# Optimization experiments

Hardware: AMD Instinct MI355X
Metric: run time of the kernel (lower is better)

## Reference

```python
import jax, jax.numpy as jnp
import numpy as np


def setup_inputs() -> dict:
    key = jax.random.key(0)
    k1, k2, k3 = jax.random.split(key, 3)
    B, Lc, Lq, D = 32, 1024, 128, 1024
    context_features = jax.random.normal(k1, (B, Lc, D), dtype=jnp.float32)
    question_features = jax.random.normal(k2, (B, Lq, D), dtype=jnp.float32)
    # weight of nn.Linear(3*D, 1, bias=False): shape (3*D,), split into w1,w2,w3
    w = jax.random.normal(k3, (3 * D,), dtype=jnp.float32) * (1.0 / np.sqrt(3 * D))
    return {"context_features": context_features, "question_features": question_features, "w": w}


def reference(context_features, question_features, w):
    B, Lc, D = context_features.shape
    Lq = question_features.shape[1]
    w1, w2, w3 = w[:D], w[D:2 * D], w[2 * D:]
    # Trilinear similarity: sim[b,i,j] = w1.c_i + w2.q_j + w3.(c_i*q_j)
    # Decomposed so the (B,Lc,Lq,3D) concat tensor is never materialized.
    sim = (
        jnp.einsum("bcd,d->bc", context_features, w1)[:, :, None]      # [B,Lc,1]
        + jnp.einsum("bqd,d->bq", question_features, w2)[:, None, :]    # [B,1,Lq]
        + jnp.einsum("bcd,bqd->bcq", context_features * w3, question_features)
    )  # [B,Lc,Lq]
    # context-to-question attention
    c2q = jnp.einsum("bcq,bqd->bcd", jax.nn.softmax(sim, axis=2), question_features)
    # question-to-context attention
    b = jax.nn.softmax(jnp.max(sim, axis=2), axis=-1)                   # [B,Lc]
    q2c = jnp.einsum("bc,bcd->bd", b, context_features)                 # [B,D]
    q2c = jnp.broadcast_to(q2c[:, None, :], (B, Lc, D))                 # repeat over Lc
    return (c2q, q2c)
```

## Files before the change

kernel.cpp:

```cpp
#include <hip/hip_runtime.h>
#include <hip/hip_bf16.h>
#include <stdint.h>

#define B_  32
#define LC  1024
#define LQ  128
#define DD  1024
#define CT  64
#define BK  64

typedef __attribute__((ext_vector_type(8))) short short8;
typedef __attribute__((ext_vector_type(4))) float f4;
typedef unsigned short u16;

__device__ __forceinline__ u16 f2bf(float f) {
  __hip_bfloat16 h = __float2bfloat16(f);
  return *reinterpret_cast<u16*>(&h);
}

__device__ __forceinline__ void gld16(const u16* g, void* l) {
  __builtin_amdgcn_global_load_lds(
      (const __attribute__((address_space(1))) unsigned int*)g,
      (__attribute__((address_space(3))) unsigned int*)l,
      16, 0, 0);
}

__device__ __forceinline__ void barrier_vm4() {
  __builtin_amdgcn_sched_barrier(0);
  asm volatile("s_waitcnt vmcnt(4) lgkmcnt(0)" ::: "memory");
  __builtin_amdgcn_s_barrier();
  __builtin_amdgcn_sched_barrier(0);
}

__global__ __launch_bounds__(256) void k1m(const float* __restrict__ qf,
                                           const float* __restrict__ w,
                                           u16* __restrict__ qw3_bf,
                                           u16* __restrict__ qT_bf,
                                           float* __restrict__ qwpart) {
  __shared__ float w3s[128];
  __shared__ float w2s[128];
  __shared__ __align__(16) u16 ldsq[128][136];
  int blk = blockIdx.x;
  int b = blk >> 3, dt = blk & 7;
  int t = threadIdx.x;
  if (t < 128) { w3s[t] = w[2 * DD + dt * 128 + t]; w2s[t] = w[DD + dt * 128 + t]; }
  __syncthreads();
  {
    int q = t >> 1, half = t & 1;
    const float* src = qf + (size_t)(b * LQ + q) * DD + dt * 128 + half * 64;
    u16* dst = qw3_bf + (size_t)(b * LQ + q) * DD + dt * 128 + half * 64;
    float s2 = 0.f;
    #pragma unroll
    for (int j = 0; j < 8; ++j) {
      float4 a = *(const float4*)(src + j * 8);
      float4 c = *(const float4*)(src + j * 8 + 4);
      float vals[8] = {a.x, a.y, a.z, a.w, c.x, c.y, c.z, c.w};
      u16 u3[8] __attribute__((aligned(16)));
      #pragma unroll
      for (int jj = 0; jj < 8; ++jj) {
        int dl = half * 64 + j * 8 + jj;
        s2 += vals[jj] * w2s[dl];
        u3[jj] = f2bf(vals[jj] * w3s[dl]);
        ldsq[dl][q] = f2bf(vals[jj]);
      }
      *(short8*)(dst + j * 8) = *(short8*)u3;
    }
    s2 += __shfl_xor(s2, 1);
    if (half == 0) qwpart[(size_t)(b * 8 + dt) * LQ + q] = s2;
  }
  __syncthreads();
  {
    int d = t >> 1, qh = (t & 1) * 64;
    u16* gdst = qT_bf + (size_t)b * DD * LQ + (size_t)(dt * 128 + d) * LQ + qh;
    #pragma unroll
    for (int i = 0; i < 8; ++i) {
      short8 v = *(const short8*)(&ldsq[d][qh + i * 8]);
      *(short8*)(gdst + i * 8) = v;
    }
  }
}

__device__ __forceinline__ void stage3(const u16* aqT, int dt,
                                       unsigned char* qbase, int wv, int lane) {
  #pragma unroll
  for (int i = 0; i < 4; ++i) {
    unsigned rel = wv * 4096 + i * 1024 + lane * 16;
    int r = rel >> 8, c = (rel >> 4) & 15, cs = c ^ (r & 7);
    gld16(aqT + (size_t)(dt * 64 + r) * LQ + cs * 8, qbase + wv * 4096 + i * 1024);
  }
}

#define STAGEB_PH1(K0, BUF)                                                    \
  do {                                                                         \
    _Pragma("unroll")                                                          \
    for (int i_ = 0; i_ < 4; ++i_) {                                           \
      unsigned rel_ = wv * 4096 + i_ * 1024 + lane * 16;                       \
      int r_ = rel_ >> 7, c_ = (rel_ >> 4) & 7, cs_ = c_ ^ (r_ & 7);           \
      gld16(aq3 + (size_t)r_ * DD + (K0) + cs_ * 8,                            \
            (BUF) + 8192 + wv * 4096 + i_ * 1024);                             \
    }                                                                          \
  } while (0)

#define LOADCTX_PH1(VA, K0)                                                    \
  do {                                                                         \
    const float* s_ = actx + (size_t)ar * DD + (K0) + akc;                     \
    *(float4*)(VA)      = *(const float4*)(s_);                                \
    *(float4*)(VA + 4)  = *(const float4*)(s_ + 4);                            \
    *(float4*)(VA + 8)  = *(const float4*)(s_ + 8);                            \
    *(float4*)(VA + 12) = *(const float4*)(s_ + 12);                           \
  } while (0)

#define CWWRITE_PH1(VA, K0, BUF)                                               \
  do {                                                                         \
    _Pragma("unroll")                                                          \
    for (int j_ = 0; j_ < 4; ++j_) {                                           \
      float4 w4_ = *(const float4*)(&w1s[(K0) + akc + j_ * 4]);                \
      cwp += (VA)[j_ * 4 + 0] * w4_.x + (VA)[j_ * 4 + 1] * w4_.y +             \
             (VA)[j_ * 4 + 2] * w4_.z + (VA)[j_ * 4 + 3] * w4_.w;              \
    }                                                                          \
    {                                                                          \
      u16 u_[16] __attribute__((aligned(16)));                                 \
      _Pragma("unroll")                                                        \
      for (int j_ = 0; j_ < 16; ++j_) u_[j_] = f2bf((VA)[j_]);                 \
      int cu_ = akc >> 3;                                                      \
      *(short8*)((BUF) + ar * 128 + ((cu_ ^ (ar & 7)) << 4)) = *(short8*)u_;   \
      *(short8*)((BUF) + ar * 128 + (((cu_ + 1) ^ (ar & 7)) << 4)) =           \
          *(short8*)(u_ + 8);                                                  \
    }                                                                          \
  } while (0)

#define MFMA_PH1(BUFC)                                                         \
  do {                                                                         \
    _Pragma("unroll")                                                          \
    for (int kk = 0; kk < 2; ++kk) {                                           \
      short8 afr[2], bfr[4];                                                   \
      _Pragma("unroll")                                                        \
      for (int m_ = 0; m_ < 2; ++m_) {                                         \
        int r_ = wr * 32 + m_ * 16 + l15;                                      \
        int byte_ = r_ * 128 + kk * 64 + l4 * 16;                              \
        byte_ ^= (r_ & 7) << 4;                                                \
        afr[m_] = *(const short8*)((BUFC) + byte_);                            \
      }                                                                        \
      _Pragma("unroll")                                                        \
      for (int n_ = 0; n_ < 4; ++n_) {                                         \
        int r_ = wc * 64 + n_ * 16 + l15;                                      \
        int byte_ = r_ * 128 + kk * 64 + l4 * 16;                              \
        byte_ ^= (r_ & 7) << 4;                                                \
        bfr[n_] = *(const short8*)((BUFC) + 8192 + byte_);                     \
      }                                                                        \
      _Pragma("unroll")                                                        \
      for (int m_ = 0; m_ < 2; ++m_)                                           \
        _Pragma("unroll")                                                      \
        for (int n_ = 0; n_ < 4; ++n_)                                         \
          acc[m_][n_] = __builtin_amdgcn_mfma_f32_16x16x32_bf16(               \
              afr[m_], bfr[n_], acc[m_][n_], 0, 0, 0);                         \
    }                                                                          \
  } while (0)

#define PH1_ITER(T, VA_WR, VA_LD, BUFC, BUFN)                                  \
  do {                                                                         \
    STAGEB_PH1(((T) + 1) * BK, BUFN);                                          \
    __builtin_amdgcn_sched_barrier(0);                                         \
    LOADCTX_PH1(VA_LD, ((T) + 2) * BK);                                        \
    MFMA_PH1(BUFC);                                                            \
    CWWRITE_PH1(VA_WR, ((T) + 1) * BK, BUFN);                                  \
    barrier_vm4();                                                             \
  } while (0)

__global__ __launch_bounds__(256, 2) void kA(const float* __restrict__ ctx,
                                          const u16* __restrict__ qw3_bf,
                                          const u16* __restrict__ qT_bf,
                                          const float* __restrict__ w,
                                          const float* __restrict__ qwpart,
                                          float* __restrict__ c2q,
                                          float* __restrict__ partial,
                                          float* __restrict__ tileM,
                                          float* __restrict__ tileS) {
  __shared__ __align__(16) unsigned char tile[49152];
  __shared__ __align__(16) float w1s[DD];
  __shared__ float cws[CT];
  __shared__ float qws[LQ];
  __shared__ float rm2[2][CT];
  __shared__ float rs2[2][CT];
  __shared__ float rmax[CT];
  __shared__ float rinv[CT];
  __shared__ float wgtl[CT];

  unsigned char* psm = tile + 32768;

  const int tid = threadIdx.x;
  const int bid = blockIdx.x;
  const int blk = (bid & 7) * 64 + (bid >> 3);
  const int b   = blk >> 4;
  const int c0  = (blk & 15) * CT;
  const int lane = tid & 63;
  const int wv   = tid >> 6;
  const int wr   = wv >> 1;
  const int wc   = wv & 1;
  const int l15  = lane & 15;
  const int l4   = lane >> 4;

  *(f4*)(&w1s[tid * 4]) = *(const f4*)(w + tid * 4);
  if (tid < LQ) {
    float s = 0.f;
    #pragma unroll
    for (int dt = 0; dt < 8; ++dt) s += qwpart[(size_t)(b * 8 + dt) * LQ + tid];
    qws[tid] = s;
  }

  f4 acc[2][4];
  #pragma unroll
  for (int m = 0; m < 2; ++m)
    #pragma unroll
    for (int n = 0; n < 4; ++n) { f4 z = {0.f, 0.f, 0.f, 0.f}; acc[m][n] = z; }

  const float* actx = ctx + (size_t)(b * LC + c0) * DD;
  const u16* aq3  = qw3_bf + (size_t)b * LQ * DD;
  const u16* aqT  = qT_bf + (size_t)b * DD * LQ;

  const int ar  = tid >> 2;
  const int akc = (tid & 3) * 16;

  float vaA[16], vaB[16];
  float cwp = 0.f;

  __syncthreads();

  {
    LOADCTX_PH1(vaA, 0);
    __builtin_amdgcn_sched_barrier(0);
    STAGEB_PH1(0, tile);
    __builtin_amdgcn_sched_barrier(0);
    CWWRITE_PH1(vaA, 0, tile);
    LOADCTX_PH1(vaB, BK);
    barrier_vm4();
  }

  for (int t2 = 0; t2 < 7; ++t2) {
    PH1_ITER(2 * t2,     vaB, vaA, tile,         tile + 24576);
    PH1_ITER(2 * t2 + 1, vaA, vaB, tile + 24576, tile);
  }
  {
    STAGEB_PH1(15 * BK, tile + 24576);
    MFMA_PH1(tile);
    CWWRITE_PH1(vaB, 15 * BK, tile + 24576);
    __syncthreads();
  }
  MFMA_PH1(tile + 24576);
  __syncthreads();

  cwp += __shfl_xor(cwp, 1);
  cwp += __shfl_xor(cwp, 2);
  if ((lane & 3) == 0) cws[ar] = cwp;
  __syncthreads();

  #pragma unroll
  for (int m = 0; m < 2; ++m) {
    #pragma unroll
    for (int j = 0; j < 4; ++j) {
      int cl = wr * 32 + m * 16 + l4 * 4 + j;
      float mx = -1e30f;
      #pragma unroll
      for (int n = 0; n < 4; ++n) {
        float v = acc[m][n][j] + cws[cl] + qws[wc * 64 + n * 16 + l15];
        acc[m][n][j] = v;
        mx = fmaxf(mx, v);
      }
      #pragma unroll
      for (int off = 1; off < 16; off <<= 1) mx = fmaxf(mx, __shfl_xor(mx, off));
      if (l15 == 0) rm2[wc][cl] = mx;
    }
  }
  __syncthreads();
  if (tid < CT) rmax[tid] = fmaxf(rm2[0][tid], rm2[1][tid]);
  __syncthreads();
  #pragma unroll
  for (int m = 0; m < 2; ++m) {
    #pragma unroll
    for (int j = 0; j < 4; ++j) {
      int cl = wr * 32 + m * 16 + l4 * 4 + j;
      float mx = rmax[cl];
      float s = 0.f;
      #pragma unroll
      for (int n = 0; n < 4; ++n) {
        float p = __expf(acc[m][n][j] - mx);
        s += p;
        int q = wc * 64 + n * 16 + l15;
        int byte = cl * (LQ * 2) + q * 2;
        byte ^= (cl & 7) << 4;
        *(u16*)(psm + byte) = f2bf(p);
      }
      #pragma unroll
      for (int off = 1; off < 16; off <<= 1) s += __shfl_xor(s, off);
      if (l15 == 0) rs2[wc][cl] = s;
    }
  }
  __syncthreads();
  if (tid < CT) {
    rinv[tid] = 1.f / (rs2[0][tid] + rs2[1][tid]);
    float m = rmax[tid];
    float M = m;
    #pragma unroll
    for (int off = 32; off; off >>= 1) M = fmaxf(M, __shfl_xor(M, off));
    float wq = __expf(m - M);
    wgtl[tid] = wq;
    float S = wq;
    #pragma unroll
    for (int off = 32; off; off >>= 1) S += __shfl_xor(S, off);
    if (tid == 0) { tileM[blk] = M; tileS[blk] = S; }
  }
  __syncthreads();

  stage3(aqT, 0, tile, wv, lane);
  __syncthreads();

  float ri[2];
  ri[0] = rinv[wr * 32 + l15];
  ri[1] = rinv[wr * 32 + 16 + l15];

  f4 pacc25 = {0.f, 0.f, 0.f, 0.f};
  const float* pbase = actx + tid * 4;

  for (int dt = 0; dt < 16; ++dt) {
    int cur = dt & 1;
    if (dt < 15) stage3(aqT, dt + 1, tile + (cur ^ 1) * 16384, wv, lane);
    #pragma unroll
    for (int cc = 0; cc < 4; ++cc) {
      int c = dt * 4 + cc;
      pacc25 += wgtl[c] * *(const f4*)(pbase + (size_t)c * DD);
    }
    unsigned char* qbase = tile + cur * 16384;
    f4 pacc[2][2];
    #pragma unroll
    for (int n = 0; n < 2; ++n)
      #pragma unroll
      for (int m = 0; m < 2; ++m) { f4 z = {0.f, 0.f, 0.f, 0.f}; pacc[n][m] = z; }
    #pragma unroll
    for (int kk = 0; kk < 4; ++kk) {
      short8 pa[2], qb[2];
      #pragma unroll
      for (int m = 0; m < 2; ++m) {
        int r = wr * 32 + m * 16 + l15;
        int byte = r * 256 + kk * 64 + l4 * 16;
        byte ^= (r & 7) << 4;
        pa[m] = *(const short8*)(psm + byte);
      }
      #pragma unroll
      for (int n = 0; n < 2; ++n) {
        int dl = wc * 32 + n * 16 + l15;
        int byte = dl * 256 + kk * 64 + l4 * 16;
        byte ^= (dl & 7) << 4;
        qb[n] = *(const short8*)(qbase + byte);
      }
      #pragma unroll
      for (int n = 0; n < 2; ++n)
        #pragma unroll
        for (int m = 0; m < 2; ++m)
          pacc[n][m] = __builtin_amdgcn_mfma_f32_16x16x32_bf16(qb[n], pa[m], pacc[n][m], 0, 0, 0);
    }
    #pragma unroll
    for (int n = 0; n < 2; ++n)
      #pragma unroll
      for (int m = 0; m < 2; ++m) {
        f4 v = pacc[n][m] * ri[m];
        int cl = wr * 32 + m * 16 + l15;
        int dc = wc * 32 + n * 16 + l4 * 4;
        *(f4*)(c2q + (size_t)(b * LC + c0 + cl) * DD + dt * 64 + dc) = v;
      }
    __syncthreads();
  }

  *(f4*)(partial + (size_t)blk * DD + tid * 4) = pacc25;
}

__global__ __launch_bounds__(256) void kQC2(const float* __restrict__ partial,
                                            const float* __restrict__ tileM,
                                            const float* __restrict__ tileS,
                                            float* __restrict__ out2) {
  int blk = blockIdx.x;
  int b = blk >> 5, cb = blk & 31;
  int t = threadIdx.x;
  __shared__ float sc[16];
  __shared__ float dninv;
  if (t < 16) {
    float m = tileM[b * 16 + t];
    float M = m;
    #pragma unroll
    for (int off = 8; off; off >>= 1) M = fmaxf(M, __shfl_xor(M, off));
    float e = __expf(m - M);
    sc[t] = e;
    float d = e * tileS[b * 16 + t];
    #pragma unroll
    for (int off = 8; off; off >>= 1) d += __shfl_xor(d, off);
    if (t == 0) dninv = 1.f / d;
  }
  __syncthreads();
  f4 a = {0.f, 0.f, 0.f, 0.f};
  #pragma unroll
  for (int i = 0; i < 16; ++i) {
    float s = sc[i];
    f4 v = *(const f4*)(partial + (size_t)(b * 16 + i) * DD + t * 4);
    a += s * v;
  }
  a *= dninv;
  float* dst = out2 + ((size_t)b * LC + cb * 32) * DD + t * 4;
  #pragma unroll
  for (int r = 0; r < 32; ++r) *(f4*)(dst + (size_t)r * DD) = a;
}

extern "C" void kernel_launch(void* const* d_in, const int* in_sizes, int n_in,
                              void* d_out, int out_size, void* d_ws, size_t ws_size,
                              hipStream_t stream) {
  (void)in_sizes; (void)n_in; (void)out_size; (void)ws_size;
  const float* ctx = (const float*)d_in[0];
  const float* qf  = (const float*)d_in[1];
  const float* w   = (const float*)d_in[2];
  float* out      = (float*)d_out;
  float* c2q      = out;
  float* q2c_out  = out + (size_t)B_ * LC * DD;

  float* ws     = (float*)d_ws;
  float* qwpart = ws;
  float* tileM  = qwpart + B_ * 8 * LQ;
  float* tileS  = tileM + 512;
  float* part   = tileS + 512;
  u16*   qw3_bf = (u16*)(part + 512 * DD);
  u16*   qT_bf  = qw3_bf + (size_t)B_ * LQ * DD;

  hipLaunchKernelGGL(k1m,  dim3(256),  dim3(256), 0, stream, qf, w, qw3_bf, qT_bf, qwpart);
  hipLaunchKernelGGL(kA,   dim3(512),  dim3(256), 0, stream, ctx, qw3_bf, qT_bf, w, qwpart, c2q, part, tileM, tileS);
  hipLaunchKernelGGL(kQC2, dim3(1024), dim3(256), 0, stream, part, tileM, tileS, q2c_out);
}
```

Baseline: 136.4 us.

## Split fused attention kernel into similarity kernel and separate PV matmul kernel

```diff
diff --git a/kernel.cpp b/kernel.cpp
--- a/kernel.cpp
+++ b/kernel.cpp
@@ -23,13 +23,6 @@
       (const __attribute__((address_space(1))) unsigned int*)g,
       (__attribute__((address_space(3))) unsigned int*)l,
       16, 0, 0);
-}
-
-__device__ __forceinline__ void barrier_vm4() {
-  __builtin_amdgcn_sched_barrier(0);
-  asm volatile("s_waitcnt vmcnt(4) lgkmcnt(0)" ::: "memory");
-  __builtin_amdgcn_s_barrier();
-  __builtin_amdgcn_sched_barrier(0);
 }
 
 __global__ __launch_bounds__(256) void k1m(const float* __restrict__ qf,
@@ -77,16 +70,6 @@
       short8 v = *(const short8*)(&ldsq[d][qh + i * 8]);
       *(short8*)(gdst + i * 8) = v;
     }
-  }
-}
-
-__device__ __forceinline__ void stage3(const u16* aqT, int dt,
-                                       unsigned char* qbase, int wv, int lane) {
-  #pragma unroll
-  for (int i = 0; i < 4; ++i) {
-    unsigned rel = wv * 4096 + i * 1024 + lane * 16;
-    int r = rel >> 8, c = (rel >> 4) & 15, cs = c ^ (r & 7);
-    gld16(aqT + (size_t)(dt * 64 + r) * LQ + cs * 8, qbase + wv * 4096 + i * 1024);
   }
 }
 
@@ -157,22 +140,12 @@
     }                                                                          \
   } while (0)
 
-#define PH1_ITER(T, VA_WR, VA_LD, BUFC, BUFN)                                  \
-  do {                                                                         \
-    STAGEB_PH1(((T) + 1) * BK, BUFN);                                          \
-    __builtin_amdgcn_sched_barrier(0);                                         \
-    LOADCTX_PH1(VA_LD, ((T) + 2) * BK);                                        \
-    MFMA_PH1(BUFC);                                                            \
-    CWWRITE_PH1(VA_WR, ((T) + 1) * BK, BUFN);                                  \
-    barrier_vm4();                                                             \
-  } while (0)
-
-__global__ __launch_bounds__(256, 2) void kA(const float* __restrict__ ctx,
+__global__ __launch_bounds__(256, 2) void kSim(const float* __restrict__ ctx,
                                           const u16* __restrict__ qw3_bf,
-                                          const u16* __restrict__ qT_bf,
                                           const float* __restrict__ w,
                                           const float* __restrict__ qwpart,
-                                          float* __restrict__ c2q,
+                                          u16* __restrict__ Pg,
+                                          float* __restrict__ rinvg,
                                           float* __restrict__ partial,
                                           float* __restrict__ tileM,
                                           float* __restrict__ tileS) {
@@ -216,38 +189,36 @@
 
   const float* actx = ctx + (size_t)(b * LC + c0) * DD;
   const u16* aq3  = qw3_bf + (size_t)b * LQ * DD;
-  const u16* aqT  = qT_bf + (size_t)b * DD * LQ;
 
   const int ar  = tid >> 2;
   const int akc = (tid & 3) * 16;
 
-  float vaA[16], vaB[16];
+  float va[16];
   float cwp = 0.f;
 
   __syncthreads();
 
   {
-    LOADCTX_PH1(vaA, 0);
+    LOADCTX_PH1(va, 0);
     __builtin_amdgcn_sched_barrier(0);
     STAGEB_PH1(0, tile);
     __builtin_amdgcn_sched_barrier(0);
-    CWWRITE_PH1(vaA, 0, tile);
-    LOADCTX_PH1(vaB, BK);
-    barrier_vm4();
-  }
-
-  for (int t2 = 0; t2 < 7; ++t2) {
-    PH1_ITER(2 * t2,     vaB, vaA, tile,         tile + 24576);
-    PH1_ITER(2 * t2 + 1, vaA, vaB, tile + 24576, tile);
-  }
-  {
-    STAGEB_PH1(15 * BK, tile + 24576);
-    MFMA_PH1(tile);
-    CWWRITE_PH1(vaB, 15 * BK, tile + 24576);
+    CWWRITE_PH1(va, 0, tile);
+  }
+  __syncthreads();
+
+  for (int t = 0; t < 16; ++t) {
+    int cur = t & 1;
+    unsigned char* bufc = tile + cur * 24576;
+    unsigned char* bufn = tile + (cur ^ 1) * 24576;
+    if (t < 15) {
+      LOADCTX_PH1(va, (t + 1) * BK);
+      STAGEB_PH1((t + 1) * BK, bufn);
+    }
+    MFMA_PH1(bufc);
+    if (t < 15) CWWRITE_PH1(va, (t + 1) * BK, bufn);
     __syncthreads();
   }
-  MFMA_PH1(tile + 24576);
-  __syncthreads();
 
   cwp += __shfl_xor(cwp, 1);
   cwp += __shfl_xor(cwp, 2);
@@ -311,66 +282,90 @@
   }
   __syncthreads();
 
-  stage3(aqT, 0, tile, wv, lane);
-  __syncthreads();
+  if (tid < CT) rinvg[blk * CT + tid] = rinv[tid];
+
+  {
+    int row = tid >> 2, chunk = tid & 3;
+    u16* pg = Pg + (size_t)blk * (CT * LQ) + row * LQ + chunk * 32;
+    #pragma unroll
+    for (int j = 0; j < 4; ++j) {
+      int col16 = chunk * 4 + j;
+      int sb = row * 256 + ((col16 ^ (row & 7)) << 4);
+      short8 v = *(const short8*)(psm + sb);
+      *(short8*)(pg + j * 8) = v;
+    }
+  }
+
+  {
+    f4 pacc25 = {0.f, 0.f, 0.f, 0.f};
+    const float* pbase = actx + tid * 4;
+    #pragma unroll 8
+    for (int c = 0; c < CT; ++c)
+      pacc25 += wgtl[c] * *(const f4*)(pbase + (size_t)c * DD);
+    *(f4*)(partial + (size_t)blk * DD + tid * 4) = pacc25;
+  }
+}
+
+__global__ __launch_bounds__(256, 3) void kPV(const u16* __restrict__ Pg,
+                                              const u16* __restrict__ qT_bf,
+                                              const float* __restrict__ rinvg,
+                                              float* __restrict__ c2q) {
+  const int tid = threadIdx.x;
+  const int bid = blockIdx.x;
+  const int lb  = (bid & 7) * 512 + (bid >> 3);
+  const int blk = lb >> 3;
+  const int dch = lb & 7;
+  const int b   = blk >> 4;
+  const int c0  = (blk & 15) * CT;
+  const int lane = tid & 63;
+  const int wv   = tid >> 6;
+  const int wr   = wv >> 1;
+  const int wd   = wv & 1;
+  const int l15  = lane & 15;
+  const int l4   = lane >> 4;
+
+  const u16* pt  = Pg + (size_t)blk * (CT * LQ);
+  const u16* qb0 = qT_bf + (size_t)b * DD * LQ;
 
   float ri[2];
-  ri[0] = rinv[wr * 32 + l15];
-  ri[1] = rinv[wr * 32 + 16 + l15];
-
-  f4 pacc25 = {0.f, 0.f, 0.f, 0.f};
-  const float* pbase = actx + tid * 4;
-
-  for (int dt = 0; dt < 16; ++dt) {
-    int cur = dt & 1;
-    if (dt < 15) stage3(aqT, dt + 1, tile + (cur ^ 1) * 16384, wv, lane);
-    #pragma unroll
-    for (int cc = 0; cc < 4; ++cc) {
-      int c = dt * 4 + cc;
-      pacc25 += wgtl[c] * *(const f4*)(pbase + (size_t)c * DD);
-    }
-    unsigned char* qbase = tile + cur * 16384;
-    f4 pacc[2][2];
-    #pragma unroll
-    for (int n = 0; n < 2; ++n)
-      #pragma unroll
-      for (int m = 0; m < 2; ++m) { f4 z = {0.f, 0.f, 0.f, 0.f}; pacc[n][m] = z; }
-    #pragma unroll
-    for (int kk = 0; kk < 4; ++kk) {
-      short8 pa[2], qb[2];
-      #pragma unroll
-      for (int m = 0; m < 2; ++m) {
-        int r = wr * 32 + m * 16 + l15;
-        int byte = r * 256 + kk * 64 + l4 * 16;
-        byte ^= (r & 7) << 4;
-        pa[m] = *(const short8*)(psm + byte);
-      }
-      #pragma unroll
-      for (int n = 0; n < 2; ++n) {
-        int dl = wc * 32 + n * 16 + l15;
-        int byte = dl * 256 + kk * 64 + l4 * 16;
-        byte ^= (dl & 7) << 4;
-        qb[n] = *(const short8*)(qbase + byte);
-      }
-      #pragma unroll
-      for (int n = 0; n < 2; ++n)
-        #pragma unroll
-        for (int m = 0; m < 2; ++m)
-          pacc[n][m] = __builtin_amdgcn_mfma_f32_16x16x32_bf16(qb[n], pa[m], pacc[n][m], 0, 0, 0);
-    }
-    #pragma unroll
-    for (int n = 0; n < 2; ++n)
-      #pragma unroll
-      for (int m = 0; m < 2; ++m) {
-        f4 v = pacc[n][m] * ri[m];
-        int cl = wr * 32 + m * 16 + l15;
-        int dc = wc * 32 + n * 16 + l4 * 4;
-        *(f4*)(c2q + (size_t)(b * LC + c0 + cl) * DD + dt * 64 + dc) = v;
-      }
-    __syncthreads();
-  }
-
-  *(f4*)(partial + (size_t)blk * DD + tid * 4) = pacc25;
+  ri[0] = rinvg[blk * CT + wr * 32 + l15];
+  ri[1] = rinvg[blk * CT + wr * 32 + 16 + l15];
+
+  f4 pacc[4][2];
+  #pragma unroll
+  for (int n = 0; n < 4; ++n)
+    #pragma unroll
+    for (int m = 0; m < 2; ++m) { f4 z = {0.f, 0.f, 0.f, 0.f}; pacc[n][m] = z; }
+
+  #pragma unroll
+  for (int kk = 0; kk < 4; ++kk) {
+    short8 pa[2], qb[4];
+    #pragma unroll
+    for (int m = 0; m < 2; ++m) {
+      int r = wr * 32 + m * 16 + l15;
+      pa[m] = *(const short8*)(pt + (size_t)r * LQ + kk * 32 + l4 * 8);
+    }
+    #pragma unroll
+    for (int n = 0; n < 4; ++n) {
+      int dl = dch * 128 + wd * 64 + n * 16 + l15;
+      qb[n] = *(const short8*)(qb0 + (size_t)dl * LQ + kk * 32 + l4 * 8);
+    }
+    #pragma unroll
+    for (int n = 0; n < 4; ++n)
+      #pragma unroll
+      for (int m = 0; m < 2; ++m)
+        pacc[n][m] = __builtin_amdgcn_mfma_f32_16x16x32_bf16(qb[n], pa[m], pacc[n][m], 0, 0, 0);
+  }
+
+  #pragma unroll
+  for (int n = 0; n < 4; ++n)
+    #pragma unroll
+    for (int m = 0; m < 2; ++m) {
+      f4 v = pacc[n][m] * ri[m];
+      int cl = wr * 32 + m * 16 + l15;
+      int dc = dch * 128 + wd * 64 + n * 16 + l4 * 4;
+      *(f4*)(c2q + (size_t)(b * LC + c0 + cl) * DD + dc) = v;
+    }
 }
 
 __global__ __launch_bounds__(256) void kQC2(const float* __restrict__ partial,
@@ -423,11 +418,14 @@
   float* qwpart = ws;
   float* tileM  = qwpart + B_ * 8 * LQ;
   float* tileS  = tileM + 512;
-  float* part   = tileS + 512;
+  float* rinvg  = tileS + 512;
+  float* part   = rinvg + 512 * CT;
   u16*   qw3_bf = (u16*)(part + 512 * DD);
   u16*   qT_bf  = qw3_bf + (size_t)B_ * LQ * DD;
+  u16*   Pg     = qT_bf + (size_t)B_ * DD * LQ;
 
   hipLaunchKernelGGL(k1m,  dim3(256),  dim3(256), 0, stream, qf, w, qw3_bf, qT_bf, qwpart);
-  hipLaunchKernelGGL(kA,   dim3(512),  dim3(256), 0, stream, ctx, qw3_bf, qT_bf, w, qwpart, c2q, part, tileM, tileS);
+  hipLaunchKernelGGL(kSim, dim3(512),  dim3(256), 0, stream, ctx, qw3_bf, w, qwpart, Pg, rinvg, part, tileM, tileS);
+  hipLaunchKernelGGL(kPV,  dim3(4096), dim3(256), 0, stream, Pg, qT_bf, rinvg, c2q);
   hipLaunchKernelGGL(kQC2, dim3(1024), dim3(256), 0, stream, part, tileM, tileS, q2c_out);
 }
```

Result: slower. 160.1 us (+17.4%).

## Load context A fragments directly into MFMA registers, skipping LDS staging

Applied to the files above, without the earlier changes.

```diff
diff --git a/kernel.cpp b/kernel.cpp
--- a/kernel.cpp
+++ b/kernel.cpp
@@ -23,13 +23,6 @@
       (const __attribute__((address_space(1))) unsigned int*)g,
       (__attribute__((address_space(3))) unsigned int*)l,
       16, 0, 0);
-}
-
-__device__ __forceinline__ void barrier_vm4() {
-  __builtin_amdgcn_sched_barrier(0);
-  asm volatile("s_waitcnt vmcnt(4) lgkmcnt(0)" ::: "memory");
-  __builtin_amdgcn_s_barrier();
-  __builtin_amdgcn_sched_barrier(0);
 }
 
 __global__ __launch_bounds__(256) void k1m(const float* __restrict__ qf,
@@ -90,84 +83,73 @@
   }
 }
 
-#define STAGEB_PH1(K0, BUF)                                                    \
+#define STAGEB(K0, BUF)                                                        \
   do {                                                                         \
     _Pragma("unroll")                                                          \
     for (int i_ = 0; i_ < 4; ++i_) {                                           \
       unsigned rel_ = wv * 4096 + i_ * 1024 + lane * 16;                       \
       int r_ = rel_ >> 7, c_ = (rel_ >> 4) & 7, cs_ = c_ ^ (r_ & 7);           \
       gld16(aq3 + (size_t)r_ * DD + (K0) + cs_ * 8,                            \
-            (BUF) + 8192 + wv * 4096 + i_ * 1024);                             \
+            (BUF) + wv * 4096 + i_ * 1024);                                    \
     }                                                                          \
   } while (0)
 
-#define LOADCTX_PH1(VA, K0)                                                    \
-  do {                                                                         \
-    const float* s_ = actx + (size_t)ar * DD + (K0) + akc;                     \
-    *(float4*)(VA)      = *(const float4*)(s_);                                \
-    *(float4*)(VA + 4)  = *(const float4*)(s_ + 4);                            \
-    *(float4*)(VA + 8)  = *(const float4*)(s_ + 8);                            \
-    *(float4*)(VA + 12) = *(const float4*)(s_ + 12);                           \
-  } while (0)
-
-#define CWWRITE_PH1(VA, K0, BUF)                                               \
+#define ALOAD(K0)                                                              \
   do {                                                                         \
     _Pragma("unroll")                                                          \
-    for (int j_ = 0; j_ < 4; ++j_) {                                           \
-      float4 w4_ = *(const float4*)(&w1s[(K0) + akc + j_ * 4]);                \
-      cwp += (VA)[j_ * 4 + 0] * w4_.x + (VA)[j_ * 4 + 1] * w4_.y +             \
-             (VA)[j_ * 4 + 2] * w4_.z + (VA)[j_ * 4 + 3] * w4_.w;              \
-    }                                                                          \
-    {                                                                          \
-      u16 u_[16] __attribute__((aligned(16)));                                 \
+    for (int m_ = 0; m_ < 2; ++m_)                                             \
       _Pragma("unroll")                                                        \
-      for (int j_ = 0; j_ < 16; ++j_) u_[j_] = f2bf((VA)[j_]);                 \
-      int cu_ = akc >> 3;                                                      \
-      *(short8*)((BUF) + ar * 128 + ((cu_ ^ (ar & 7)) << 4)) = *(short8*)u_;   \
-      *(short8*)((BUF) + ar * 128 + (((cu_ + 1) ^ (ar & 7)) << 4)) =           \
-          *(short8*)(u_ + 8);                                                  \
+      for (int q_ = 0; q_ < 2; ++q_) {                                         \
+        const float* s_ = arow[m_] + (K0) + q_ * 32;                           \
+        va[m_][q_][0] = *(const float4*)(s_);                                  \
+        va[m_][q_][1] = *(const float4*)(s_ + 4);                              \
+      }                                                                        \
+  } while (0)
+
+#define ACVT(K0)                                                               \
+  do {                                                                         \
+    _Pragma("unroll")                                                          \
+    for (int q_ = 0; q_ < 2; ++q_) {                                           \
+      float4 wa_ = *(const float4*)(w + (K0) + q_ * 32 + koff);                \
+      float4 wb_ = *(const float4*)(w + (K0) + q_ * 32 + koff + 4);            \
+      _Pragma("unroll")                                                        \
+      for (int m_ = 0; m_ < 2; ++m_) {                                         \
+        cwp[m_] += va[m_][q_][0].x * wa_.x + va[m_][q_][0].y * wa_.y +         \
+                   va[m_][q_][0].z * wa_.z + va[m_][q_][0].w * wa_.w +         \
+                   va[m_][q_][1].x * wb_.x + va[m_][q_][1].y * wb_.y +         \
+                   va[m_][q_][1].z * wb_.z + va[m_][q_][1].w * wb_.w;          \
+        u16 u_[8] __attribute__((aligned(16)));                                \
+        u_[0] = f2bf(va[m_][q_][0].x); u_[1] = f2bf(va[m_][q_][0].y);          \
+        u_[2] = f2bf(va[m_][q_][0].z); u_[3] = f2bf(va[m_][q_][0].w);          \
+        u_[4] = f2bf(va[m_][q_][1].x); u_[5] = f2bf(va[m_][q_][1].y);          \
+        u_[6] = f2bf(va[m_][q_][1].z); u_[7] = f2bf(va[m_][q_][1].w);          \
+        af[m_][q_] = *(short8*)u_;                                             \
+      }                                                                        \
     }                                                                          \
   } while (0)
 
-#define MFMA_PH1(BUFC)                                                         \
+#define MFMAP1(BUFC)                                                           \
   do {                                                                         \
     _Pragma("unroll")                                                          \
     for (int kk = 0; kk < 2; ++kk) {                                           \
-      short8 afr[2], bfr[4];                                                   \
-      _Pragma("unroll")                                                        \
-      for (int m_ = 0; m_ < 2; ++m_) {                                         \
-        int r_ = wr * 32 + m_ * 16 + l15;                                      \
-        int byte_ = r_ * 128 + kk * 64 + l4 * 16;                              \
-        byte_ ^= (r_ & 7) << 4;                                                \
-        afr[m_] = *(const short8*)((BUFC) + byte_);                            \
-      }                                                                        \
+      short8 bfr[4];                                                           \
       _Pragma("unroll")                                                        \
       for (int n_ = 0; n_ < 4; ++n_) {                                         \
         int r_ = wc * 64 + n_ * 16 + l15;                                      \
         int byte_ = r_ * 128 + kk * 64 + l4 * 16;                              \
         byte_ ^= (r_ & 7) << 4;                                                \
-        bfr[n_] = *(const short8*)((BUFC) + 8192 + byte_);                     \
+        bfr[n_] = *(const short8*)((BUFC) + byte_);                            \
       }                                                                        \
       _Pragma("unroll")                                                        \
       for (int m_ = 0; m_ < 2; ++m_)                                           \
         _Pragma("unroll")                                                      \
         for (int n_ = 0; n_ < 4; ++n_)                                         \
           acc[m_][n_] = __builtin_amdgcn_mfma_f32_16x16x32_bf16(               \
-              afr[m_], bfr[n_], acc[m_][n_], 0, 0, 0);                         \
+              af[m_][kk], bfr[n_], acc[m_][n_], 0, 0, 0);                      \
     }                                                                          \
   } while (0)
 
-#define PH1_ITER(T, VA_WR, VA_LD, BUFC, BUFN)                                  \
-  do {                                                                         \
-    STAGEB_PH1(((T) + 1) * BK, BUFN);                                          \
-    __builtin_amdgcn_sched_barrier(0);                                         \
-    LOADCTX_PH1(VA_LD, ((T) + 2) * BK);                                        \
-    MFMA_PH1(BUFC);                                                            \
-    CWWRITE_PH1(VA_WR, ((T) + 1) * BK, BUFN);                                  \
-    barrier_vm4();                                                             \
-  } while (0)
-
-__global__ __launch_bounds__(256, 2) void kA(const float* __restrict__ ctx,
+__global__ __launch_bounds__(256, 3) void kA(const float* __restrict__ ctx,
                                           const u16* __restrict__ qw3_bf,
                                           const u16* __restrict__ qT_bf,
                                           const float* __restrict__ w,
@@ -177,7 +159,6 @@
                                           float* __restrict__ tileM,
                                           float* __restrict__ tileS) {
   __shared__ __align__(16) unsigned char tile[49152];
-  __shared__ __align__(16) float w1s[DD];
   __shared__ float cws[CT];
   __shared__ float qws[LQ];
   __shared__ float rm2[2][CT];
@@ -199,8 +180,8 @@
   const int wc   = wv & 1;
   const int l15  = lane & 15;
   const int l4   = lane >> 4;
-
-  *(f4*)(&w1s[tid * 4]) = *(const f4*)(w + tid * 4);
+  const int koff = l4 * 8;
+
   if (tid < LQ) {
     float s = 0.f;
     #pragma unroll
@@ -218,40 +199,42 @@
   const u16* aq3  = qw3_bf + (size_t)b * LQ * DD;
   const u16* aqT  = qT_bf + (size_t)b * DD * LQ;
 
-  const int ar  = tid >> 2;
-  const int akc = (tid & 3) * 16;
-
-  float vaA[16], vaB[16];
-  float cwp = 0.f;
-
-  __syncthreads();
-
-  {
-    LOADCTX_PH1(vaA, 0);
-    __builtin_amdgcn_sched_barrier(0);
-    STAGEB_PH1(0, tile);
-    __builtin_amdgcn_sched_barrier(0);
-    CWWRITE_PH1(vaA, 0, tile);
-    LOADCTX_PH1(vaB, BK);
-    barrier_vm4();
-  }
-
-  for (int t2 = 0; t2 < 7; ++t2) {
-    PH1_ITER(2 * t2,     vaB, vaA, tile,         tile + 24576);
-    PH1_ITER(2 * t2 + 1, vaA, vaB, tile + 24576, tile);
-  }
-  {
-    STAGEB_PH1(15 * BK, tile + 24576);
-    MFMA_PH1(tile);
-    CWWRITE_PH1(vaB, 15 * BK, tile + 24576);
+  const float* arow[2];
+  arow[0] = actx + (size_t)(wr * 32 + l15) * DD + koff;
+  arow[1] = arow[0] + (size_t)16 * DD;
+
+  float4 va[2][2][2];
+  short8 af[2][2];
+  float cwp[2] = {0.f, 0.f};
+
+  __syncthreads();
+
+  ALOAD(0);
+  STAGEB(0, tile);
+  ACVT(0);
+  __syncthreads();
+
+  for (int t = 0; t < 16; ++t) {
+    unsigned char* bufc = tile + (t & 1) * 16384;
+    unsigned char* bufn = tile + ((t & 1) ^ 1) * 16384;
+    if (t < 15) {
+      STAGEB((t + 1) * BK, bufn);
+      ALOAD((t + 1) * BK);
+    }
+    MFMAP1(bufc);
+    if (t < 15) ACVT((t + 1) * BK);
     __syncthreads();
   }
-  MFMA_PH1(tile + 24576);
-  __syncthreads();
-
-  cwp += __shfl_xor(cwp, 1);
-  cwp += __shfl_xor(cwp, 2);
-  if ((lane & 3) == 0) cws[ar] = cwp;
+
+  #pragma unroll
+  for (int m = 0; m < 2; ++m) {
+    cwp[m] += __shfl_xor(cwp[m], 16);
+    cwp[m] += __shfl_xor(cwp[m], 32);
+  }
+  if (wc == 0 && l4 == 0) {
+    cws[wr * 32 + l15]      = cwp[0];
+    cws[wr * 32 + 16 + l15] = cwp[1];
+  }
   __syncthreads();
 
   #pragma unroll
```

Result: slower. 142.9 us (+4.8%).
